# Kernel tuning notes

Measured on AMD Instinct MI355X. Metric: run time of the kernel, lower is better.

## Reference

```python
import jax, jax.numpy as jnp
import numpy as np
import math
from jax import lax

KPAD = 4  # padding for 9x9 depthwise conv (same spatial size)

def dwconv(x, w, b):
    # x: [B,C,H,W], w: [C,1,9,9] depthwise (groups=C), b: [C]
    y = lax.conv_general_dilated(
        x, w, window_strides=(1, 1), padding=[(KPAD, KPAD), (KPAD, KPAD)],
        dimension_numbers=("NCHW", "OIHW", "NCHW"), feature_group_count=x.shape[1])
    return y + b[None, :, None, None]

def channel_pos_encoding(c, h, w, dtype):
    # position over channels, frequencies over the flattened spatial dim
    hw = h * w
    position = jnp.arange(c, dtype=jnp.float32)[:, None]                  # [C,1]
    div_term = jnp.exp(jnp.arange(0, hw, 2, dtype=jnp.float32) * (-math.log(10000.0) / hw))  # [hw/2]
    ang = position * div_term                                             # [C,hw/2]
    pe = jnp.stack([jnp.sin(ang), jnp.cos(ang)], axis=-1).reshape(c, hw)  # interleave sin/cos
    return pe.reshape(c, h, w).astype(dtype)

def setup_inputs() -> dict:
    key = jax.random.key(0)
    ks = jax.random.split(key, 9)
    B, C, H, W = 4, 256, 128, 128
    x = jax.random.normal(ks[0], (B, C, H, W), dtype=jnp.float32)
    def wgt(k):
        return jax.random.normal(k, (C, 1, 9, 9), dtype=jnp.float32) * 0.1
    return {
        "x": x,
        "q_w": wgt(ks[1]), "q_b": jax.random.normal(ks[2], (C,), dtype=jnp.float32) * 0.1,
        "k_w": wgt(ks[3]), "k_b": jax.random.normal(ks[4], (C,), dtype=jnp.float32) * 0.1,
        "v_w": wgt(ks[5]), "v_b": jax.random.normal(ks[6], (C,), dtype=jnp.float32) * 0.1,
        "o_w": wgt(ks[7]), "o_b": jax.random.normal(ks[8], (C,), dtype=jnp.float32) * 0.1,
        "num_heads": 8,
    }

def reference(x, q_w, q_b, k_w, k_b, v_w, v_b, o_w, o_b, num_heads):
    b, c, h, w = x.shape
    hw = h * w
    d = hw // num_heads  # per-head spatial dim
    x = x + channel_pos_encoding(c, h, w, x.dtype)[None]
    q = dwconv(x, q_w, q_b).reshape(b, c, num_heads, d)  # [B,C,H,D]
    k = dwconv(x, k_w, k_b).reshape(b, c, num_heads, d)
    v = dwconv(x, v_w, v_b).reshape(b, c, num_heads, d)
    # channel-over-channel attention in fp32 (matches forced fp32 cast)
    qk = jnp.einsum("bqhd,bkhd->bhqk", q.astype(jnp.float32), k.astype(jnp.float32)) / math.sqrt(hw)
    attn = jax.nn.softmax(qk, axis=-1)
    a = jnp.einsum("bhqk,bkhd->bqhd", attn.astype(v.dtype), v).reshape(b, c, h, w)
    return dwconv(a, o_w, o_b)
```

## Files before the change

kernel.cpp:

```cpp
#include <hip/hip_runtime.h>
#include <hip/hip_bf16.h>
#include <math.h>

#define BB 4
#define CC 256
#define HH 128
#define WW 128
#define HWS (HH*WW)
#define NHEADS 8
#define DD (HWS/NHEADS)

typedef __attribute__((ext_vector_type(8))) short bf16x8;
typedef __attribute__((ext_vector_type(4))) float f32x4;
typedef __attribute__((ext_vector_type(2))) __fp16 h16x2;
typedef __attribute__((ext_vector_type(8))) __fp16 h16x8;

#define GLD_LDS(g, l) __builtin_amdgcn_global_load_lds( \
    (const __attribute__((address_space(1))) void*)(g),  \
    (__attribute__((address_space(3))) void*)(l), 16, 0, 0)

static __device__ __forceinline__ unsigned short f2bf(float f) {
    unsigned int u = __float_as_uint(f);
    unsigned int r = (u + 0x7FFFu + ((u >> 16) & 1u)) >> 16;
    return (unsigned short)r;
}
static __device__ __forceinline__ float b2f(unsigned short u) {
    return __uint_as_float((unsigned int)u << 16);
}
static __device__ __forceinline__ unsigned int pk2(float a, float b) {
    union { h16x2 h; unsigned int u; } x;
    x.h = __builtin_amdgcn_cvt_pkrtz(a, b);
    return x.u;
}

__global__ __launch_bounds__(256) void build_wt(
    const float* __restrict__ qw, const float* __restrict__ kw,
    const float* __restrict__ vw, unsigned short* __restrict__ wt)
{
    const int c = blockIdx.x, cv = blockIdx.y;
    const float* w = (cv == 0) ? qw : (cv == 1) ? kw : vw;
    unsigned short* dst = wt + ((size_t)c * 3 + cv) * 9 * 512;
    for (int idx = threadIdx.x; idx < 9 * 512; idx += 256) {
        const int ky   = idx >> 9;
        const int rem  = idx & 511;
        const int lane = rem >> 3, e = rem & 7;
        const int m = lane & 15;
        const int k = ((lane >> 4) << 3) + e;
        const int d = k - m;
        const float v = (d >= 0 && d <= 8) ? w[c * 81 + ky * 9 + d] : 0.0f;
        const __fp16 hv = (__fp16)v;
        unsigned short bits;
        __builtin_memcpy(&bits, &hv, 2);
        dst[idx] = bits;
    }
}

#define FOFF 27648
#define PE_COEF   (-1.1243088e-3f)
#define PE_RSTEP  (0.99887632f)
__global__ __launch_bounds__(512, 6) void conv9qkv(
    const float* __restrict__ in,
    const unsigned short* __restrict__ wt,
    const float* __restrict__ b0, const float* __restrict__ b1,
    const float* __restrict__ b2,
    unsigned short* __restrict__ o0, unsigned short* __restrict__ o1,
    unsigned short* __restrict__ o2)
{
    __shared__ alignas(16) char lds[FOFF + 21760];

    const int u    = ((blockIdx.x & 7) << 8) + (blockIdx.x >> 3);
    const int c    = u >> 3;
    const int bidx = (u >> 1) & 3;
    const int tc   = (u & 1) << 6;
    const int tid  = threadIdx.x;
    const int lane = tid & 63;
    const int wr   = tid >> 6;
    const int r16  = lane & 15;
    const int g    = lane >> 4;

    for (int f = wr; f < 27; f += 8) {
        const char* src = (const char*)wt + (((size_t)c * 27 + f) << 10) + (lane << 4);
        GLD_LDS(src, lds + (f << 10) + (lane << 4));
    }

    const float* xp = in + ((size_t)(bidx * CC + c) << 14);
    const float cf  = (float)c;

    #pragma unroll
    for (int it = 0; it < 3; ++it) {
        const int i = tid + (it << 9);
        if (i < 1360) {
            const int row = i / 10;
            const int c8  = i - row * 10;
            const int gy  = row - 4;
            const int gx  = tc + (c8 << 3) - 4;
            uint4 wv = make_uint4(0u, 0u, 0u, 0u);
            if (gy >= 0 && gy < HH) {
                const float* xr = xp + (gy << 7);
                if (gx >= 0 && gx + 7 < WW) {
                    const float4 a0 = *(const float4*)(xr + gx);
                    const float4 a1 = *(const float4*)(xr + gx + 4);
                    float dt = __expf(PE_COEF * (float)(((gy << 7) + gx) >> 1));
                    float s, cc;
                    __sincosf(cf * dt, &s, &cc);
                    wv.x = pk2(a0.x + s, a0.y + cc);
                    dt *= PE_RSTEP;
                    __sincosf(cf * dt, &s, &cc);
                    wv.y = pk2(a0.z + s, a0.w + cc);
                    dt *= PE_RSTEP;
                    __sincosf(cf * dt, &s, &cc);
                    wv.z = pk2(a1.x + s, a1.y + cc);
                    dt *= PE_RSTEP;
                    __sincosf(cf * dt, &s, &cc);
                    wv.w = pk2(a1.z + s, a1.w + cc);
                } else {
                    float vv[8];
                    #pragma unroll
                    for (int e = 0; e < 8; ++e) {
                        const int gxe = gx + e;
                        float xv = 0.f;
                        if (gxe >= 0 && gxe < WW) {
                            const int flat = (gy << 7) + gxe;
                            const float dt = __expf(PE_COEF * (float)(flat >> 1));
                            float s, cc;
                            __sincosf(cf * dt, &s, &cc);
                            xv = xr[gxe] + ((flat & 1) ? cc : s);
                        }
                        vv[e] = xv;
                    }
                    wv.x = pk2(vv[0], vv[1]); wv.y = pk2(vv[2], vv[3]);
                    wv.z = pk2(vv[4], vv[5]); wv.w = pk2(vv[6], vv[7]);
                }
            }
            int byte = row * 160 + (c8 << 4);
            byte ^= (row & 7) << 4;
            *(uint4*)(lds + FOFF + byte) = wv;
        }
    }
    __syncthreads();

    f32x4 acc[3][4];
    {
        const float bq = b0[c], bk = b1[c], bv = b2[c];
        #pragma unroll
        for (int xt = 0; xt < 4; ++xt) {
            acc[0][xt] = (f32x4){bq, bq, bq, bq};
            acc[1][xt] = (f32x4){bk, bk, bk, bk};
            acc[2][xt] = (f32x4){bv, bv, bv, bv};
        }
    }

    const int rowbase = (wr << 4) + r16;
    __builtin_amdgcn_s_setprio(1);
    for (int ky = 0; ky < 9; ++ky) {
        const int row = rowbase + ky;
        const int sx  = (row & 7) << 4;
        const int rb  = row * 160 + (g << 4);
        h16x8 a[4];
        #pragma unroll
        for (int xt = 0; xt < 4; ++xt)
            a[xt] = *(const h16x8*)(lds + FOFF + ((rb + (xt << 5)) ^ sx));
        #pragma unroll
        for (int cv = 0; cv < 3; ++cv) {
            const h16x8 tf = *(const h16x8*)(lds + ((cv * 9 + ky) << 10) + (lane << 4));
            #pragma unroll
            for (int xt = 0; xt < 4; ++xt)
                acc[cv][xt] = __builtin_amdgcn_mfma_f32_16x16x32_f16(
                    tf, a[xt], acc[cv][xt], 0, 0, 0);
        }
    }
    __builtin_amdgcn_s_setprio(0);

    unsigned short* const outs[3] = { o0, o1, o2 };
    const size_t base = (((size_t)(bidx * NHEADS + wr) * CC + c) << 11)
                      + ((size_t)r16 << 7) + tc + (g << 2);
    #pragma unroll
    for (int cv = 0; cv < 3; ++cv)
        #pragma unroll
        for (int xt = 0; xt < 4; ++xt) {
            ushort4 uo;
            uo.x = f2bf(acc[cv][xt][0]); uo.y = f2bf(acc[cv][xt][1]);
            uo.z = f2bf(acc[cv][xt][2]); uo.w = f2bf(acc[cv][xt][3]);
            *(ushort4*)(outs[cv] + base + (xt << 4)) = uo;
        }
}

#define O_FRAG_OFF 11520
__global__ __launch_bounds__(256, 7) void conv9o(
    const unsigned short* __restrict__ ain,
    const float* __restrict__ w, const float* __restrict__ b,
    float* __restrict__ out)
{
    __shared__ alignas(16) char lds[O_FRAG_OFF + 9216];
    __shared__ float lw[81];

    const int u    = ((blockIdx.x & 7) << 9) + (blockIdx.x >> 3);
    const int c    = u >> 4;
    const int bidx = (u >> 2) & 3;
    const int t    = u & 3;
    const int plane = bidx * CC + c;
    const int tr   = (t >> 1) << 6;
    const int tc   = (t & 1) << 6;
    const int tid  = threadIdx.x;
    const int lane = tid & 63;
    const int wr   = tid >> 6;
    const int r16  = lane & 15;
    const int g    = lane >> 4;

    if (tid < 81) lw[tid] = w[c * 81 + tid];

    const unsigned short* ap = ain + (size_t)plane * HWS;

    #pragma unroll
    for (int it = 0; it < 3; ++it) {
        const int i = tid + (it << 8);
        if (i < 720) {
            const int row = i / 10;
            const int c8  = i - row * 10;
            const int gy  = tr + row - 4;
            const int gx  = tc + (c8 << 3) - 4;
            uint4 wv = make_uint4(0u, 0u, 0u, 0u);
            if (gy >= 0 && gy < HH) {
                const unsigned short* ar = ap + (gy << 7);
                if (gx >= 0 && gx + 7 < WW) {
                    const bf16x8 uu = *(const bf16x8*)(ar + gx);
                    wv.x = pk2(b2f((unsigned short)uu[0]), b2f((unsigned short)uu[1]));
                    wv.y = pk2(b2f((unsigned short)uu[2]), b2f((unsigned short)uu[3]));
                    wv.z = pk2(b2f((unsigned short)uu[4]), b2f((unsigned short)uu[5]));
                    wv.w = pk2(b2f((unsigned short)uu[6]), b2f((unsigned short)uu[7]));
                } else {
                    float vv[8];
                    #pragma unroll
                    for (int e = 0; e < 8; ++e) {
                        const int gxe = gx + e;
                        vv[e] = (gxe >= 0 && gxe < WW) ? b2f(ar[gxe]) : 0.f;
                    }
                    wv.x = pk2(vv[0], vv[1]); wv.y = pk2(vv[2], vv[3]);
                    wv.z = pk2(vv[4], vv[5]); wv.w = pk2(vv[6], vv[7]);
                }
            }
            int byte = row * 160 + (c8 << 4);
            byte ^= (row & 7) << 4;
            *(uint4*)(lds + byte) = wv;
        }
    }
    __syncthreads();

    {
        const int ln = tid >> 2, qq = tid & 3;
        const int m  = ln & 15;
        const int k0 = ((ln >> 4) << 3) + (qq << 1);
        const int d0 = k0 - m, d1 = k0 + 1 - m;
        #pragma unroll
        for (int ky = 0; ky < 9; ++ky) {
            const float f0 = (d0 >= 0 && d0 <= 8) ? lw[ky * 9 + d0] : 0.f;
            const float f1 = (d1 >= 0 && d1 <= 8) ? lw[ky * 9 + d1] : 0.f;
            *(unsigned int*)(lds + O_FRAG_OFF + (ky << 10) + (ln << 4) + (qq << 2)) = pk2(f0, f1);
        }
    }
    __syncthreads();

    const float bv = b[c];
    f32x4 acc[4];
    #pragma unroll
    for (int xt = 0; xt < 4; ++xt) acc[xt] = (f32x4){bv, bv, bv, bv};

    const int rowbase = (wr << 4) + r16;
    __builtin_amdgcn_s_setprio(1);
    for (int ky = 0; ky < 9; ++ky) {
        const int row = rowbase + ky;
        const int sx  = (row & 7) << 4;
        const int rb  = row * 160 + (g << 4);
        h16x8 a[4];
        #pragma unroll
        for (int xt = 0; xt < 4; ++xt)
            a[xt] = *(const h16x8*)(lds + ((rb + (xt << 5)) ^ sx));
        const h16x8 tf = *(const h16x8*)(lds + O_FRAG_OFF + (ky << 10) + (lane << 4));
        #pragma unroll
        for (int xt = 0; xt < 4; ++xt)
            acc[xt] = __builtin_amdgcn_mfma_f32_16x16x32_f16(tf, a[xt], acc[xt], 0, 0, 0);
    }
    __builtin_amdgcn_s_setprio(0);

    const int y = tr + (wr << 4) + r16;
    float* orow = out + (size_t)plane * HWS + (size_t)y * WW + tc + (g << 2);
    #pragma unroll
    for (int xt = 0; xt < 4; ++xt)
        *(f32x4*)(orow + (xt << 4)) = acc[xt];
}

__global__ __launch_bounds__(256) void transpose_v(
    const unsigned short* __restrict__ v, unsigned short* __restrict__ vT)
{
    __shared__ unsigned short t[64][72];

    const int bh = blockIdx.z;
    const int c0 = blockIdx.y << 6;
    const int d0 = blockIdx.x << 6;
    const int tid = threadIdx.x;
    const int r  = tid >> 2;
    const int q4 = tid & 3;

    const unsigned short* src = v + (size_t)bh * CC * DD + (size_t)(c0 + r) * DD + d0 + q4 * 16;
    bf16x8 v0 = *(const bf16x8*)(src);
    bf16x8 v1 = *(const bf16x8*)(src + 8);
    #pragma unroll
    for (int e = 0; e < 8; ++e) {
        t[q4 * 16 + e][r]     = (unsigned short)v0[e];
        t[q4 * 16 + 8 + e][r] = (unsigned short)v1[e];
    }
    __syncthreads();

    unsigned short* dst = vT + (size_t)bh * DD * CC + (size_t)(d0 + r) * CC + c0 + q4 * 16;
    *(bf16x8*)dst       = *(const bf16x8*)&t[r][q4 * 16];
    *(bf16x8*)(dst + 8) = *(const bf16x8*)&t[r][q4 * 16 + 8];
}

template<bool IS_QK>
__global__ __launch_bounds__(256) void gemm_bf16(
    const unsigned short* __restrict__ Abuf, const unsigned short* __restrict__ Bbuf,
    void* __restrict__ Dout)
{
    constexpr int KT = IS_QK ? 2048 : 256;
    constexpr int NB = IS_QK ? 256 : 2048;

    __shared__ char lds[24576];

    const int tid = threadIdx.x;
    const int bh  = blockIdx.z;
    const int m0  = blockIdx.y << 7;
    const int n0  = blockIdx.x << 6;

    const unsigned short* Ab = Abuf + (size_t)bh * CC * KT + (size_t)m0 * KT;
    const unsigned short* Bb = Bbuf + (size_t)bh * NB * KT + (size_t)n0 * KT;

    const int lane = tid & 63;
    const int w    = tid >> 6;
    const int wm   = (w >> 1) << 6;
    const int wn   = (w & 1) << 5;
    const int r16  = lane & 15;
    const int g    = lane >> 4;

    const int trow = tid >> 3;
    const int slot = tid & 7;

    f32x4 acc[4][2] = {};

    for (int kt = 0; kt < KT / 64; ++kt) {
        const int kc = kt << 6;
        #pragma unroll
        for (int i = 0; i < 4; ++i) {
            const int row = (i << 5) + trow;
            const int gs  = slot ^ (row & 7);
            const char* srcp = (const char*)(Ab + (size_t)row * KT + kc) + gs * 16;
            GLD_LDS(srcp, lds + (i << 12) + tid * 16);
        }
        #pragma unroll
        for (int i = 0; i < 2; ++i) {
            const int row = (i << 5) + trow;
            const int gs  = slot ^ (row & 7);
            const char* srcp = (const char*)(Bb + (size_t)row * KT + kc) + gs * 16;
            GLD_LDS(srcp, lds + 16384 + (i << 12) + tid * 16);
        }
        __syncthreads();
        #pragma unroll
        for (int kk = 0; kk < 2; ++kk) {
            bf16x8 af[4], bfr[2];
            #pragma unroll
            for (int mi = 0; mi < 4; ++mi) {
                const int row = wm + (mi << 4) + r16;
                af[mi] = *(const bf16x8*)(lds + row * 128 + ((((kk << 2) + g) ^ (row & 7)) << 4));
            }
            #pragma unroll
            for (int nj = 0; nj < 2; ++nj) {
                const int row = wn + (nj << 4) + r16;
                bfr[nj] = *(const bf16x8*)(lds + 16384 + row * 128 + ((((kk << 2) + g) ^ (row & 7)) << 4));
            }
            #pragma unroll
            for (int mi = 0; mi < 4; ++mi)
                #pragma unroll
                for (int nj = 0; nj < 2; ++nj)
                    acc[mi][nj] = __builtin_amdgcn_mfma_f32_16x16x32_bf16(af[mi], bfr[nj], acc[mi][nj], 0, 0, 0);
        }
        __syncthreads();
    }

    if (IS_QK) {
        float* sp = (float*)Dout + (size_t)bh * 65536;
        #pragma unroll
        for (int mi = 0; mi < 4; ++mi)
            #pragma unroll
            for (int nj = 0; nj < 2; ++nj)
                #pragma unroll
                for (int j = 0; j < 4; ++j) {
                    const int row = m0 + wm + (mi << 4) + (g << 2) + j;
                    const int col = n0 + wn + (nj << 4) + r16;
                    sp[(size_t)row * 256 + col] = acc[mi][nj][j] * 0.0078125f;
                }
    } else {
        unsigned short* Ao = (unsigned short*)Dout;
        const int b = bh >> 3, h = bh & 7;
        #pragma unroll
        for (int mi = 0; mi < 4; ++mi)
            #pragma unroll
            for (int nj = 0; nj < 2; ++nj)
                #pragma unroll
                for (int j = 0; j < 4; ++j) {
                    const int row = m0 + wm + (mi << 4) + (g << 2) + j;
                    const int col = n0 + wn + (nj << 4) + r16;
                    Ao[((size_t)b * CC + row) * HWS + h * DD + col] = f2bf(acc[mi][nj][j]);
                }
    }
}

__global__ __launch_bounds__(256) void softmax_kernel(
    const float* __restrict__ S, __hip_bfloat16* __restrict__ P)
{
    __shared__ float redm[4], reds[4];
    const int row = blockIdx.x;
    const float* p = S + (size_t)row * 256;
    const int tid = threadIdx.x;
    float vv = p[tid];
    float m = vv;
    #pragma unroll
    for (int o = 32; o; o >>= 1) m = fmaxf(m, __shfl_xor(m, o, 64));
    if ((tid & 63) == 0) redm[tid >> 6] = m;
    __syncthreads();
    m = fmaxf(fmaxf(redm[0], redm[1]), fmaxf(redm[2], redm[3]));
    const float e = expf(vv - m);
    float s = e;
    #pragma unroll
    for (int o = 32; o; o >>= 1) s += __shfl_xor(s, o, 64);
    if ((tid & 63) == 0) reds[tid >> 6] = s;
    __syncthreads();
    s = reds[0] + reds[1] + reds[2] + reds[3];
    P[(size_t)row * 256 + tid] = __float2bfloat16(e / s);
}

extern "C" void kernel_launch(void* const* d_in, const int* in_sizes, int n_in,
                              void* d_out, int out_size, void* d_ws, size_t ws_size,
                              hipStream_t stream)
{
    const float* x  = (const float*)d_in[0];
    const float* qw = (const float*)d_in[1];
    const float* qb = (const float*)d_in[2];
    const float* kw = (const float*)d_in[3];
    const float* kb = (const float*)d_in[4];
    const float* vw = (const float*)d_in[5];
    const float* vb = (const float*)d_in[6];
    const float* ow = (const float*)d_in[7];
    const float* ob = (const float*)d_in[8];
    float* out = (float*)d_out;

    char* wsb = (char*)d_ws;
    __hip_bfloat16* q   = (__hip_bfloat16*)(wsb + 16777216UL);
    __hip_bfloat16* k   = (__hip_bfloat16*)(wsb + 50331648UL);
    float*          S   = (float*)(wsb + 83886080UL);
    __hip_bfloat16* P   = (__hip_bfloat16*)(wsb + 92274688UL);
    __hip_bfloat16* v   = (__hip_bfloat16*)(wsb + 96468992UL);
    __hip_bfloat16* vT  = (__hip_bfloat16*)(wsb + 130023424UL);
    unsigned short* A   = (unsigned short*)(wsb + 0);
    unsigned short* wt  = (unsigned short*)(wsb + 83886080UL);

    build_wt<<<dim3(CC, 3), 256, 0, stream>>>(qw, kw, vw, wt);
    conv9qkv<<<dim3(CC * 8), 512, 0, stream>>>(
        x, wt, qb, kb, vb,
        (unsigned short*)q, (unsigned short*)k, (unsigned short*)v);
    gemm_bf16<true><<<dim3(4, 2, 32), 256, 0, stream>>>(
        (const unsigned short*)q, (const unsigned short*)k, (void*)S);
    softmax_kernel<<<dim3(32 * 256), 256, 0, stream>>>(S, P);
    transpose_v<<<dim3(DD / 64, CC / 64, 32), 256, 0, stream>>>(
        (const unsigned short*)v, (unsigned short*)vT);
    gemm_bf16<false><<<dim3(32, 2, 32), 256, 0, stream>>>(
        (const unsigned short*)P, (const unsigned short*)vT, (void*)A);
    conv9o<<<dim3(BB * CC * 4), 256, 0, stream>>>(A, ow, ob, out);
}
```

Before: 175.1 us.

## Fuse V transpose into PV GEMM and vectorize softmax with one wave per row

Removes the separate transpose_v kernel by having a new PV GEMM load the V tile (all 256 channels by 64 spatial columns) directly from the untransposed layout and scatter it transposed into swizzled LDS. This drops the vT intermediate and one launch. Softmax now handles a row per wavefront with float4 loads, no LDS reductions and fast exp. The trade-off is scalar 2-byte LDS stores with possible bank conflicts, and a larger LDS footprint that may lower occupancy.

```diff
diff --git a/kernel.cpp b/kernel.cpp
--- a/kernel.cpp
+++ b/kernel.cpp
@@ -289,40 +289,12 @@
         *(f32x4*)(orow + (xt << 4)) = acc[xt];
 }
 
-__global__ __launch_bounds__(256) void transpose_v(
-    const unsigned short* __restrict__ v, unsigned short* __restrict__ vT)
-{
-    __shared__ unsigned short t[64][72];
-
-    const int bh = blockIdx.z;
-    const int c0 = blockIdx.y << 6;
-    const int d0 = blockIdx.x << 6;
-    const int tid = threadIdx.x;
-    const int r  = tid >> 2;
-    const int q4 = tid & 3;
-
-    const unsigned short* src = v + (size_t)bh * CC * DD + (size_t)(c0 + r) * DD + d0 + q4 * 16;
-    bf16x8 v0 = *(const bf16x8*)(src);
-    bf16x8 v1 = *(const bf16x8*)(src + 8);
-    #pragma unroll
-    for (int e = 0; e < 8; ++e) {
-        t[q4 * 16 + e][r]     = (unsigned short)v0[e];
-        t[q4 * 16 + 8 + e][r] = (unsigned short)v1[e];
-    }
-    __syncthreads();
-
-    unsigned short* dst = vT + (size_t)bh * DD * CC + (size_t)(d0 + r) * CC + c0 + q4 * 16;
-    *(bf16x8*)dst       = *(const bf16x8*)&t[r][q4 * 16];
-    *(bf16x8*)(dst + 8) = *(const bf16x8*)&t[r][q4 * 16 + 8];
-}
-
 template<bool IS_QK>
 __global__ __launch_bounds__(256) void gemm_bf16(
     const unsigned short* __restrict__ Abuf, const unsigned short* __restrict__ Bbuf,
     void* __restrict__ Dout)
 {
-    constexpr int KT = IS_QK ? 2048 : 256;
-    constexpr int NB = IS_QK ? 256 : 2048;
+    constexpr int KT = 2048;
 
     __shared__ char lds[24576];
 
@@ -332,7 +304,7 @@
     const int n0  = blockIdx.x << 6;
 
     const unsigned short* Ab = Abuf + (size_t)bh * CC * KT + (size_t)m0 * KT;
-    const unsigned short* Bb = Bbuf + (size_t)bh * NB * KT + (size_t)n0 * KT;
+    const unsigned short* Bb = Bbuf + (size_t)bh * CC * KT + (size_t)n0 * KT;
 
     const int lane = tid & 63;
     const int w    = tid >> 6;
@@ -385,56 +357,142 @@
         __syncthreads();
     }
 
-    if (IS_QK) {
-        float* sp = (float*)Dout + (size_t)bh * 65536;
-        #pragma unroll
-        for (int mi = 0; mi < 4; ++mi)
-            #pragma unroll
-            for (int nj = 0; nj < 2; ++nj)
+    float* sp = (float*)Dout + (size_t)bh * 65536;
+    #pragma unroll
+    for (int mi = 0; mi < 4; ++mi)
+        #pragma unroll
+        for (int nj = 0; nj < 2; ++nj)
+            #pragma unroll
+            for (int j = 0; j < 4; ++j) {
+                const int row = m0 + wm + (mi << 4) + (g << 2) + j;
+                const int col = n0 + wn + (nj << 4) + r16;
+                sp[(size_t)row * 256 + col] = acc[mi][nj][j] * 0.0078125f;
+            }
+}
+
+__global__ __launch_bounds__(256) void softmax_kernel(
+    const float* __restrict__ S, unsigned short* __restrict__ P)
+{
+    const int row  = (blockIdx.x << 2) + (threadIdx.x >> 6);
+    const int lane = threadIdx.x & 63;
+    const float4 vv = *(const float4*)(S + ((size_t)row << 8) + (lane << 2));
+    float m = fmaxf(fmaxf(vv.x, vv.y), fmaxf(vv.z, vv.w));
+    #pragma unroll
+    for (int o = 32; o; o >>= 1) m = fmaxf(m, __shfl_xor(m, o, 64));
+    const float e0 = __expf(vv.x - m), e1 = __expf(vv.y - m);
+    const float e2 = __expf(vv.z - m), e3 = __expf(vv.w - m);
+    float s = (e0 + e1) + (e2 + e3);
+    #pragma unroll
+    for (int o = 32; o; o >>= 1) s += __shfl_xor(s, o, 64);
+    const float r = 1.0f / s;
+    ushort4 u;
+    u.x = f2bf(e0 * r); u.y = f2bf(e1 * r); u.z = f2bf(e2 * r); u.w = f2bf(e3 * r);
+    *(ushort4*)(P + ((size_t)row << 8) + (lane << 2)) = u;
+}
+
+__global__ __launch_bounds__(256) void gemm_pv(
+    const unsigned short* __restrict__ Pbuf, const unsigned short* __restrict__ vbuf,
+    unsigned short* __restrict__ Ao)
+{
+    __shared__ alignas(16) char lds[49152];
+
+    const int tid = threadIdx.x;
+    const int bh  = blockIdx.z;
+    const int m0  = blockIdx.y << 7;
+    const int n0  = blockIdx.x << 6;
+
+    const unsigned short* Ab = Pbuf + ((size_t)bh << 16) + ((size_t)m0 << 8);
+
+    const int lane = tid & 63;
+    const int w    = tid >> 6;
+    const int wm   = (w >> 1) << 6;
+    const int wn   = (w & 1) << 5;
+    const int r16  = lane & 15;
+    const int g    = lane >> 4;
+    const int trow = tid >> 3;
+    const int slot = tid & 7;
+
+    {
+        #pragma unroll
+        for (int i = 0; i < 4; ++i) {
+            const int row = (i << 5) + trow;
+            const int gs  = slot ^ (row & 7);
+            GLD_LDS((const char*)(Ab + (size_t)row * 256) + gs * 16,
+                    lds + (i << 12) + tid * 16);
+        }
+    }
+
+    {
+        const unsigned short* Vb = vbuf + (size_t)bh * (CC * DD) + n0;
+        const int rl = tid >> 2, q4 = tid & 3;
+        #pragma unroll
+        for (int p = 0; p < 4; ++p) {
+            const int cp = (p << 6) + rl;
+            const unsigned short* src = Vb + (size_t)cp * DD + (q4 << 4);
+            const bf16x8 v0 = *(const bf16x8*)(src);
+            const bf16x8 v1 = *(const bf16x8*)(src + 8);
+            const int cb = cp << 1;
+            #pragma unroll
+            for (int e = 0; e < 8; ++e) {
+                const int d0 = (q4 << 4) + e, d1 = d0 + 8;
+                *(unsigned short*)(lds + 16384 + d0 * 512 +
+                    (cb ^ (((d0 & 7) ^ (d0 >> 3)) << 4))) = (unsigned short)v0[e];
+                *(unsigned short*)(lds + 16384 + d1 * 512 +
+                    (cb ^ (((d1 & 7) ^ (d1 >> 3)) << 4))) = (unsigned short)v1[e];
+            }
+        }
+    }
+    __syncthreads();
+
+    f32x4 acc[4][2] = {};
+
+    for (int kt = 0; kt < 4; ++kt) {
+        #pragma unroll
+        for (int kk = 0; kk < 2; ++kk) {
+            bf16x8 af[4], bfr[2];
+            #pragma unroll
+            for (int mi = 0; mi < 4; ++mi) {
+                const int row = wm + (mi << 4) + r16;
+                af[mi] = *(const bf16x8*)(lds + row * 128 + ((((kk << 2) + g) ^ (row & 7)) << 4));
+            }
+            #pragma unroll
+            for (int nj = 0; nj < 2; ++nj) {
+                const int d = wn + (nj << 4) + r16;
+                const int kbyte = (kt << 7) + ((((kk << 2) + g)) << 4);
+                bfr[nj] = *(const bf16x8*)(lds + 16384 + d * 512 +
+                    (kbyte ^ (((d & 7) ^ (d >> 3)) << 4)));
+            }
+            #pragma unroll
+            for (int mi = 0; mi < 4; ++mi)
                 #pragma unroll
-                for (int j = 0; j < 4; ++j) {
-                    const int row = m0 + wm + (mi << 4) + (g << 2) + j;
-                    const int col = n0 + wn + (nj << 4) + r16;
-                    sp[(size_t)row * 256 + col] = acc[mi][nj][j] * 0.0078125f;
-                }
-    } else {
-        unsigned short* Ao = (unsigned short*)Dout;
-        const int b = bh >> 3, h = bh & 7;
-        #pragma unroll
-        for (int mi = 0; mi < 4; ++mi)
-            #pragma unroll
-            for (int nj = 0; nj < 2; ++nj)
-                #pragma unroll
-                for (int j = 0; j < 4; ++j) {
-                    const int row = m0 + wm + (mi << 4) + (g << 2) + j;
-                    const int col = n0 + wn + (nj << 4) + r16;
-                    Ao[((size_t)b * CC + row) * HWS + h * DD + col] = f2bf(acc[mi][nj][j]);
-                }
-    }
-}
-
-__global__ __launch_bounds__(256) void softmax_kernel(
-    const float* __restrict__ S, __hip_bfloat16* __restrict__ P)
-{
-    __shared__ float redm[4], reds[4];
-    const int row = blockIdx.x;
-    const float* p = S + (size_t)row * 256;
-    const int tid = threadIdx.x;
-    float vv = p[tid];
-    float m = vv;
-    #pragma unroll
-    for (int o = 32; o; o >>= 1) m = fmaxf(m, __shfl_xor(m, o, 64));
-    if ((tid & 63) == 0) redm[tid >> 6] = m;
-    __syncthreads();
-    m = fmaxf(fmaxf(redm[0], redm[1]), fmaxf(redm[2], redm[3]));
-    const float e = expf(vv - m);
-    float s = e;
-    #pragma unroll
-    for (int o = 32; o; o >>= 1) s += __shfl_xor(s, o, 64);
-    if ((tid & 63) == 0) reds[tid >> 6] = s;
-    __syncthreads();
-    s = reds[0] + reds[1] + reds[2] + reds[3];
-    P[(size_t)row * 256 + tid] = __float2bfloat16(e / s);
+                for (int nj = 0; nj < 2; ++nj)
+                    acc[mi][nj] = __builtin_amdgcn_mfma_f32_16x16x32_bf16(af[mi], bfr[nj], acc[mi][nj], 0, 0, 0);
+        }
+        if (kt < 3) {
+            __syncthreads();
+            const int kc = (kt + 1) << 6;
+            #pragma unroll
+            for (int i = 0; i < 4; ++i) {
+                const int row = (i << 5) + trow;
+                const int gs  = slot ^ (row & 7);
+                GLD_LDS((const char*)(Ab + (size_t)row * 256 + kc) + gs * 16,
+                        lds + (i << 12) + tid * 16);
+            }
+            __syncthreads();
+        }
+    }
+
+    const int b = bh >> 3, h = bh & 7;
+    #pragma unroll
+    for (int mi = 0; mi < 4; ++mi)
+        #pragma unroll
+        for (int nj = 0; nj < 2; ++nj)
+            #pragma unroll
+            for (int j = 0; j < 4; ++j) {
+                const int row = m0 + wm + (mi << 4) + (g << 2) + j;
+                const int col = n0 + wn + (nj << 4) + r16;
+                Ao[((size_t)b * CC + row) * HWS + h * DD + col] = f2bf(acc[mi][nj][j]);
+            }
 }
 
 extern "C" void kernel_launch(void* const* d_in, const int* in_sizes, int n_in,
@@ -458,7 +516,6 @@
     float*          S   = (float*)(wsb + 83886080UL);
     __hip_bfloat16* P   = (__hip_bfloat16*)(wsb + 92274688UL);
     __hip_bfloat16* v   = (__hip_bfloat16*)(wsb + 96468992UL);
-    __hip_bfloat16* vT  = (__hip_bfloat16*)(wsb + 130023424UL);
     unsigned short* A   = (unsigned short*)(wsb + 0);
     unsigned short* wt  = (unsigned short*)(wsb + 83886080UL);
 
@@ -468,10 +525,8 @@
         (unsigned short*)q, (unsigned short*)k, (unsigned short*)v);
     gemm_bf16<true><<<dim3(4, 2, 32), 256, 0, stream>>>(
         (const unsigned short*)q, (const unsigned short*)k, (void*)S);
-    softmax_kernel<<<dim3(32 * 256), 256, 0, stream>>>(S, P);
-    transpose_v<<<dim3(DD / 64, CC / 64, 32), 256, 0, stream>>>(
-        (const unsigned short*)v, (unsigned short*)vT);
-    gemm_bf16<false><<<dim3(32, 2, 32), 256, 0, stream>>>(
-        (const unsigned short*)P, (const unsigned short*)vT, (void*)A);
+    softmax_kernel<<<dim3(2048), 256, 0, stream>>>(S, (unsigned short*)P);
+    gemm_pv<<<dim3(32, 2, 32), 256, 0, stream>>>(
+        (const unsigned short*)P, (const unsigned short*)v, A);
     conv9o<<<dim3(BB * CC * 4), 256, 0, stream>>>(A, ow, ob, out);
 }
```

Result: faster. 150.4 us (-14.1%).
